# Performance work log

Hardware: AMD Instinct MI355X
Metric: run time of the kernel (lower is better)

The kernel has to match this reference:

```python
import jax, jax.numpy as jnp
import numpy as np

DIM = 256
H = W = 56
WS = 7           # window size
SHIFT = 3        # shift size
NH = 8           # num heads
HD = DIM // NH   # head dim
N = WS * WS      # tokens per window
SCALE = HD ** -0.5
EPS = 1e-5


def _rel_pos_index():
    coords = np.stack(np.meshgrid(np.arange(WS), np.arange(WS), indexing='ij'))  # (2,WS,WS)
    cf = coords.reshape(2, -1)                                # (2, N)
    rel = cf[:, :, None] - cf[:, None, :]                     # (2, N, N)
    rel = rel.transpose(1, 2, 0).astype(np.int64)             # (N, N, 2)
    rel[:, :, 0] += WS - 1
    rel[:, :, 1] += WS - 1
    rel[:, :, 0] *= 2 * WS - 1
    return rel.sum(-1)                                        # (N, N)

REL_IDX = _rel_pos_index()


def _attn_mask():
    # standard Swin shift mask: (nW, N, N) with 0 / -100
    img = np.zeros((H, W))
    cnt = 0
    for hs in (slice(0, -WS), slice(-WS, -SHIFT), slice(-SHIFT, None)):
        for ws in (slice(0, -WS), slice(-WS, -SHIFT), slice(-SHIFT, None)):
            img[hs, ws] = cnt
            cnt += 1
    win = img.reshape(H // WS, WS, W // WS, WS).transpose(0, 2, 1, 3).reshape(-1, N)  # (nW, N)
    diff = win[:, None, :] - win[:, :, None]
    return np.where(diff != 0, -100.0, 0.0).astype(np.float32)

ATTN_MASK = jnp.asarray(_attn_mask())  # (nW, N, N)


def _ln(x, g, b):
    mu = jnp.mean(x, -1, keepdims=True)
    var = jnp.mean(jnp.square(x - mu), -1, keepdims=True)
    return (x - mu) * jax.lax.rsqrt(var + EPS) * g + b


def _win_part(x):
    # (B,H,W,C) -> (B*nW, N, C)
    B, _, _, C = x.shape
    x = x.reshape(B, H // WS, WS, W // WS, WS, C)
    return x.transpose(0, 1, 3, 2, 4, 5).reshape(-1, N, C)


def _win_rev(xw, B):
    # (B*nW, N, C) -> (B,H,W,C)
    C = xw.shape[-1]
    x = xw.reshape(B, H // WS, W // WS, WS, WS, C)
    return x.transpose(0, 1, 3, 2, 4, 5).reshape(B, H, W, C)


def setup_inputs() -> dict:
    key = jax.random.key(0)
    ks = jax.random.split(key, 6)
    return {
        'x': jax.random.normal(ks[0], (32, H * W, DIM), jnp.float32),
        'norm1_g': jnp.ones((DIM,), jnp.float32),
        'norm1_b': jnp.zeros((DIM,), jnp.float32),
        'qkv_w': jax.random.normal(ks[1], (3 * DIM, DIM), jnp.float32) * 0.02,
        'qkv_b': jnp.zeros((3 * DIM,), jnp.float32),
        'rel_table': jax.random.normal(ks[2], ((2 * WS - 1) ** 2, NH), jnp.float32) * 0.02,
        'proj_w': jax.random.normal(ks[3], (DIM, DIM), jnp.float32) * 0.02,
        'proj_b': jnp.zeros((DIM,), jnp.float32),
        'norm2_g': jnp.ones((DIM,), jnp.float32),
        'norm2_b': jnp.zeros((DIM,), jnp.float32),
        'fc1_w': jax.random.normal(ks[4], (4 * DIM, DIM), jnp.float32) * 0.02,
        'fc1_b': jnp.zeros((4 * DIM,), jnp.float32),
        'fc2_w': jax.random.normal(ks[5], (DIM, 4 * DIM), jnp.float32) * 0.02,
        'fc2_b': jnp.zeros((DIM,), jnp.float32),
    }


def reference(x, norm1_g, norm1_b, qkv_w, qkv_b, rel_table, proj_w, proj_b,
              norm2_g, norm2_b, fc1_w, fc1_b, fc2_w, fc2_b):
    B = x.shape[0]
    shortcut = x
    h = _ln(x, norm1_g, norm1_b).reshape(B, H, W, DIM)
    # cyclic shift
    h = jnp.roll(h, (-SHIFT, -SHIFT), axis=(1, 2))
    xw = _win_part(h)                                  # (B*nW, N, C)
    Bw = xw.shape[0]
    qkv = (xw @ qkv_w.T + qkv_b).reshape(Bw, N, 3, NH, HD).transpose(2, 0, 3, 1, 4)
    q, k, v = qkv[0] * SCALE, qkv[1], qkv[2]           # (Bw, NH, N, HD)
    attn = jnp.einsum('bhnd,bhmd->bhnm', q, k)         # (Bw, NH, N, N)
    bias = rel_table[REL_IDX.reshape(-1)].reshape(N, N, NH).transpose(2, 0, 1)
    attn = attn + bias[None]
    nW = ATTN_MASK.shape[0]
    attn = attn.reshape(B, nW, NH, N, N) + ATTN_MASK[None, :, None]
    attn = jax.nn.softmax(attn.reshape(Bw, NH, N, N), axis=-1)
    out = jnp.einsum('bhnm,bhmd->bhnd', attn, v).transpose(0, 2, 1, 3).reshape(Bw, N, DIM)
    out = out @ proj_w.T + proj_b
    h = _win_rev(out, B)
    h = jnp.roll(h, (SHIFT, SHIFT), axis=(1, 2)).reshape(B, H * W, DIM)
    x = shortcut + h
    y = _ln(x, norm2_g, norm2_b)
    y = jax.nn.gelu(y @ fc1_w.T + fc1_b, approximate=False)
    y = y @ fc2_w.T + fc2_b
    return x + y
```

## Files before the change

### kernel.cpp

```cpp
#include <hip/hip_runtime.h>


typedef float f4 __attribute__((ext_vector_type(4)));
typedef __bf16 b8 __attribute__((ext_vector_type(8)));

#define DEV static __device__ __forceinline__

DEV ushort f2bf(float f) {
  union { float f; unsigned u; } c; c.f = f;
  unsigned u = c.u;
  u += 0x7fffu + ((u >> 16) & 1u);
  return (ushort)(u >> 16);
}
DEV __bf16 bfb(ushort u) { union { ushort u; __bf16 b; } c; c.u = u; return c.b; }
DEV b8 zero_b8() {
  b8 z;
#pragma unroll
  for (int i = 0; i < 8; ++i) z[i] = (__bf16)0.f;
  return z;
}
DEV void load_lds16(const void* g, void* l) {
  __builtin_amdgcn_global_load_lds(
      (const __attribute__((address_space(1))) unsigned int*)g,
      (__attribute__((address_space(3))) unsigned int*)l, 16, 0, 0);
}
DEV int reg3(int t) { return t < 49 ? 0 : (t < 53 ? 1 : 2); }

__global__ __launch_bounds__(256) void cast_w(const float* a, ushort* oa, int na,
                                              const float* b, ushort* ob, int nb,
                                              const float* c, ushort* oc, int nc,
                                              const float* d, ushort* od, int nd) {
  int total = na + nb + nc + nd;
  for (int i = blockIdx.x * 256 + threadIdx.x; i < total; i += gridDim.x * 256) {
    int j = i;
    if (j < na) { oa[j] = f2bf(a[j]); continue; }
    j -= na;
    if (j < nb) { ob[j] = f2bf(b[j]); continue; }
    j -= nb;
    if (j < nc) { oc[j] = f2bf(c[j]); continue; }
    j -= nc;
    od[j] = f2bf(d[j]);
  }
}

__global__ __launch_bounds__(256) void build_bias(const float* __restrict__ rel_table,
                                                  float* __restrict__ comb) {
  const int idx = blockIdx.x * 256 + threadIdx.x;
  if (idx >= 4 * 8 * 64 * 64) return;
  const int j = idx & 63, i = (idx >> 6) & 63, h = (idx >> 12) & 7, ty = idx >> 15;
  float v;
  if (i < 49 && j < 49) {
    const int iy = i / 7, ix = i - iy * 7, jy = j / 7, jx = j - jy * 7;
    const int ridx = (iy - jy + 6) * 13 + (ix - jx + 6);
    v = rel_table[ridx * 8 + h];
    const int wh = (ty & 2) ? 7 : 0, ww = (ty & 1) ? 7 : 0;
    const int irg = reg3(wh * 7 + iy) * 3 + reg3(ww * 7 + ix);
    const int jrg = reg3(wh * 7 + jy) * 3 + reg3(ww * 7 + jx);
    if (irg != jrg) v -= 100.f;
  } else {
    v = -1e30f;
  }
  comb[idx] = v;
}

__global__ __launch_bounds__(256) void ln_shift(const float* __restrict__ x,
                                                const float* __restrict__ g,
                                                const float* __restrict__ bta,
                                                ushort* __restrict__ out, int shifted) {
  const int wid = threadIdx.x >> 6, lane = threadIdx.x & 63;
  const int t = blockIdx.x * 4 + wid;
  int src;
  if (shifted) {
    int win = t / 49, n = t - win * 49;
    int bb = win >> 6, wh = (win >> 3) & 7, ww = win & 7;
    int wy = n / 7, wx = n - wy * 7;
    int r = wh * 7 + wy + 3; if (r >= 56) r -= 56;
    int c = ww * 7 + wx + 3; if (c >= 56) c -= 56;
    src = bb * 3136 + r * 56 + c;
  } else {
    src = t;
  }
  const float4 v = *(const float4*)(x + (size_t)src * 256 + lane * 4);
  float s  = v.x + v.y + v.z + v.w;
  float s2 = v.x * v.x + v.y * v.y + v.z * v.z + v.w * v.w;
#pragma unroll
  for (int m = 32; m; m >>= 1) { s += __shfl_xor(s, m); s2 += __shfl_xor(s2, m); }
  const float mean = s * (1.f / 256.f);
  const float var  = s2 * (1.f / 256.f) - mean * mean;
  const float rs   = rsqrtf(var + 1e-5f);
  const float4 gv = *(const float4*)(g + lane * 4);
  const float4 bv = *(const float4*)(bta + lane * 4);
  ushort4 o;
  o.x = f2bf((v.x - mean) * rs * gv.x + bv.x);
  o.y = f2bf((v.y - mean) * rs * gv.y + bv.y);
  o.z = f2bf((v.z - mean) * rs * gv.z + bv.z);
  o.w = f2bf((v.w - mean) * rs * gv.w + bv.w);
  *(ushort4*)(out + (size_t)t * 256 + lane * 4) = o;
}

template <class Epi>
__global__ __launch_bounds__(256) void gemm_bt(const ushort* __restrict__ A,
                                               const ushort* __restrict__ B,
                                               int K, int NT, Epi epi) {
  __shared__ ushort lsA[3][128 * 32];
  __shared__ ushort lsB[3][128 * 32];
  const int tid = threadIdx.x;
  const int lane = tid & 63, wid = tid >> 6;
  const int quad = lane >> 4, l16 = lane & 15;
  const int wm = wid >> 1, wn = wid & 1;
  const int lin = blockIdx.x;
  const int xcd = lin & 7, j = lin >> 3;
  const int mt = xcd * 98 + j / NT;
  const int nt_ = j % NT;
  const long rowA0 = (long)mt * 128;
  const long colB0 = (long)nt_ * 128;
  f4 acc[4][4];
#pragma unroll
  for (int i = 0; i < 4; ++i)
#pragma unroll
    for (int jj = 0; jj < 4; ++jj) { acc[i][jj][0] = 0.f; acc[i][jj][1] = 0.f; acc[i][jj][2] = 0.f; acc[i][jj][3] = 0.f; }
  const int lrow = lane >> 2;
  const int lk = ((lane & 3) ^ ((lane >> 3) & 3)) * 8;
  const int rsw = (quad ^ ((l16 >> 1) & 3)) * 8;
  const int seg0 = wid * 2, seg1 = wid * 2 + 1;
  const long ga0 = (rowA0 + seg0 * 16 + lrow) * (long)K + lk;
  const long ga1 = (rowA0 + seg1 * 16 + lrow) * (long)K + lk;
  const long gb0 = (colB0 + seg0 * 16 + lrow) * (long)K + lk;
  const long gb1 = (colB0 + seg1 * 16 + lrow) * (long)K + lk;

  const int nsteps = K >> 5;
#pragma unroll
  for (int p = 0; p < 3; ++p) {
    const int kk = p << 5;
    load_lds16(A + ga0 + kk, &lsA[p][seg0 * 512]);
    load_lds16(A + ga1 + kk, &lsA[p][seg1 * 512]);
    load_lds16(B + gb0 + kk, &lsB[p][seg0 * 512]);
    load_lds16(B + gb1 + kk, &lsB[p][seg1 * 512]);
  }
  asm volatile("s_waitcnt vmcnt(8)" ::: "memory");
  __builtin_amdgcn_s_barrier();

  int cur = 0;
  for (int t = 0; t < nsteps; ++t) {
    b8 af[4], bfr[4];
#pragma unroll
    for (int ti = 0; ti < 4; ++ti)
      af[ti] = *(const b8*)&lsA[cur][(wm * 64 + ti * 16 + l16) * 32 + rsw];
#pragma unroll
    for (int tj = 0; tj < 4; ++tj)
      bfr[tj] = *(const b8*)&lsB[cur][(wn * 64 + tj * 16 + l16) * 32 + rsw];
#pragma unroll
    for (int ti = 0; ti < 4; ++ti)
#pragma unroll
      for (int tj = 0; tj < 4; ++tj)
        acc[ti][tj] = __builtin_amdgcn_mfma_f32_16x16x32_bf16(af[ti], bfr[tj], acc[ti][tj], 0, 0, 0);
    __builtin_amdgcn_s_barrier();
    if (t + 3 < nsteps) {
      const int kk = (t + 3) << 5;
      load_lds16(A + ga0 + kk, &lsA[cur][seg0 * 512]);
      load_lds16(A + ga1 + kk, &lsA[cur][seg1 * 512]);
      load_lds16(B + gb0 + kk, &lsB[cur][seg0 * 512]);
      load_lds16(B + gb1 + kk, &lsB[cur][seg1 * 512]);
      asm volatile("s_waitcnt vmcnt(8)" ::: "memory");
    } else if (t + 2 < nsteps) {
      asm volatile("s_waitcnt vmcnt(4)" ::: "memory");
    } else if (t + 1 < nsteps) {
      asm volatile("s_waitcnt vmcnt(0)" ::: "memory");
    }
    __builtin_amdgcn_s_barrier();
    cur = cur == 2 ? 0 : cur + 1;
  }
#pragma unroll
  for (int ti = 0; ti < 4; ++ti)
#pragma unroll
    for (int tj = 0; tj < 4; ++tj)
#pragma unroll
      for (int r = 0; r < 4; ++r)
        epi((int)(rowA0 + wm * 64 + ti * 16 + quad * 4 + r),
            (int)(colB0 + wn * 64 + tj * 16 + l16), acc[ti][tj][r]);
}

struct QkvEpi {
  ushort* out; const float* bias;
  __device__ void operator()(int r, int c, float v) const {
    v += bias[c];
    if (c < 256) v *= 0.17677669529663687f;
    out[(size_t)r * 768 + c] = f2bf(v);
  }
};
struct GeluEpi {
  ushort* out; const float* bias;
  __device__ void operator()(int r, int c, float v) const {
    v += bias[c];
    v = 0.5f * v * (1.f + erff(v * 0.70710678118654752f));
    out[(size_t)r * 1024 + c] = f2bf(v);
  }
};
struct Fc2Epi {
  float* out; const float* bias;
  __device__ void operator()(int r, int c, float v) const {
    size_t i = (size_t)r * 256 + c;
    out[i] = out[i] + v + bias[c];
  }
};

__global__ __launch_bounds__(512) void attn_proj(const ushort* __restrict__ qkv,
                                                 const float* __restrict__ comb,
                                                 const ushort* __restrict__ projw,
                                                 const float* __restrict__ projb,
                                                 const float* __restrict__ x_in,
                                                 const float* __restrict__ n2g,
                                                 const float* __restrict__ n2b,
                                                 float* __restrict__ x_out,
                                                 ushort* __restrict__ xw2) {
  __shared__ ushort sbuf[32768];
  const int win = blockIdx.x;
  const int b = win >> 6, wh = (win >> 3) & 7, ww = win & 7;
  const int tid = threadIdx.x, lane = tid & 63, h = tid >> 6;
  const int quad = lane >> 4, l16 = lane & 15;
  const size_t wbase = (size_t)win * 49 * 768;

  b8 af[4], bfr[4];
#pragma unroll
  for (int ti = 0; ti < 4; ++ti) {
    const int tok = ti * 16 + l16;
    af[ti] = (tok < 49) ? *(const b8*)(qkv + wbase + (size_t)tok * 768 + h * 32 + quad * 8)
                        : zero_b8();
  }
#pragma unroll
  for (int tj = 0; tj < 4; ++tj) {
    const int key = tj * 16 + l16;
    bfr[tj] = (key < 49) ? *(const b8*)(qkv + wbase + (size_t)key * 768 + 256 + h * 32 + quad * 8)
                         : zero_b8();
  }
  f4 S[4][4];
#pragma unroll
  for (int ti = 0; ti < 4; ++ti)
#pragma unroll
    for (int tj = 0; tj < 4; ++tj) {
      S[ti][tj][0] = 0.f; S[ti][tj][1] = 0.f; S[ti][tj][2] = 0.f; S[ti][tj][3] = 0.f;
      S[ti][tj] = __builtin_amdgcn_mfma_f32_16x16x32_bf16(af[ti], bfr[tj], S[ti][tj], 0, 0, 0);
    }

  ushort* P = sbuf + h * 4096;
  const float* cmb = comb + ((((wh == 7) ? 2 : 0) + ((ww == 7) ? 1 : 0)) * 8 + h) * 4096;
#pragma unroll
  for (int ti = 0; ti < 4; ++ti) {
#pragma unroll
    for (int r = 0; r < 4; ++r) {
      const int i = ti * 16 + quad * 4 + r;
      const float* crow = cmb + i * 64 + l16;
      float sv[4];
#pragma unroll
      for (int tj = 0; tj < 4; ++tj) sv[tj] = S[ti][tj][r] + crow[tj * 16];
      float m = fmaxf(fmaxf(sv[0], sv[1]), fmaxf(sv[2], sv[3]));
#pragma unroll
      for (int d = 1; d < 16; d <<= 1) m = fmaxf(m, __shfl_xor(m, d));
      float sum = 0.f;
#pragma unroll
      for (int tj = 0; tj < 4; ++tj) { sv[tj] = __expf(sv[tj] - m); sum += sv[tj]; }
#pragma unroll
      for (int d = 1; d < 16; d <<= 1) sum += __shfl_xor(sum, d);
      const float inv = 1.f / sum;
      const int swz = i & 7, off = l16 & 7, cb = l16 >> 3;
#pragma unroll
      for (int tj = 0; tj < 4; ++tj) {
        const int cc = tj * 2 + cb;
        P[i * 64 + (((cc ^ swz) << 3) | off)] = f2bf(sv[tj] * inv);
      }
    }
  }

  f4 O[4][2];
#pragma unroll
  for (int ti = 0; ti < 4; ++ti)
#pragma unroll
    for (int tn = 0; tn < 2; ++tn) { O[ti][tn][0] = 0.f; O[ti][tn][1] = 0.f; O[ti][tn][2] = 0.f; O[ti][tn][3] = 0.f; }
#pragma unroll
  for (int kt = 0; kt < 2; ++kt) {
    b8 vb[2];
#pragma unroll
    for (int tn = 0; tn < 2; ++tn)
#pragma unroll
      for (int j = 0; j < 8; ++j) {
        const int key = kt * 32 + quad * 8 + j;
        vb[tn][j] = (key < 49)
            ? bfb(qkv[wbase + (size_t)key * 768 + 512 + h * 32 + tn * 16 + l16])
            : (__bf16)0.f;
      }
#pragma unroll
    for (int ti = 0; ti < 4; ++ti) {
      const int row = ti * 16 + l16;
      const b8 pa = *(const b8*)(P + row * 64 + (((kt * 4 + quad) ^ (row & 7)) << 3));
#pragma unroll
      for (int tn = 0; tn < 2; ++tn)
        O[ti][tn] = __builtin_amdgcn_mfma_f32_16x16x32_bf16(pa, vb[tn], O[ti][tn], 0, 0, 0);
    }
  }

  __syncthreads();
  ushort* ob = sbuf;
#pragma unroll
  for (int ti = 0; ti < 4; ++ti)
#pragma unroll
    for (int tn = 0; tn < 2; ++tn)
#pragma unroll
      for (int r = 0; r < 4; ++r) {
        const int tok = ti * 16 + quad * 4 + r;
        const int cc = h * 4 + tn * 2 + (l16 >> 3);
        ob[tok * 256 + (((cc ^ (tok & 7)) << 3) | (l16 & 7))] = f2bf(O[ti][tn][r]);
      }
  __syncthreads();

  f4 C[4][2];
#pragma unroll
  for (int ti = 0; ti < 4; ++ti)
#pragma unroll
    for (int tn = 0; tn < 2; ++tn) { C[ti][tn][0] = 0.f; C[ti][tn][1] = 0.f; C[ti][tn][2] = 0.f; C[ti][tn][3] = 0.f; }
  for (int k0 = 0; k0 < 256; k0 += 32) {
    b8 bw[2];
#pragma unroll
    for (int tn = 0; tn < 2; ++tn)
      bw[tn] = *(const b8*)(projw + (size_t)(h * 32 + tn * 16 + l16) * 256 + k0 + quad * 8);
#pragma unroll
    for (int ti = 0; ti < 4; ++ti) {
      const int row = ti * 16 + l16;
      const b8 pa = *(const b8*)(ob + row * 256 + ((((k0 >> 3) + quad) ^ (row & 7)) << 3));
#pragma unroll
      for (int tn = 0; tn < 2; ++tn)
        C[ti][tn] = __builtin_amdgcn_mfma_f32_16x16x32_bf16(pa, bw[tn], C[ti][tn], 0, 0, 0);
    }
  }

  __syncthreads();
  float* fbuf = (float*)sbuf;
#pragma unroll
  for (int ti = 0; ti < 4; ++ti)
#pragma unroll
    for (int r = 0; r < 4; ++r) {
      const int tok = ti * 16 + quad * 4 + r;
      const int swz = tok & 7;
#pragma unroll
      for (int tn = 0; tn < 2; ++tn) {
        const int c4 = h * 8 + tn * 4 + (l16 >> 2);
        fbuf[tok * 256 + (((c4 ^ swz) << 2) | (l16 & 3))] = C[ti][tn][r];
      }
    }
  __syncthreads();

  for (int t = h; t < 49; t += 8) {
    const int wy = t / 7, wx = t - wy * 7;
    int rr = wh * 7 + wy + 3; if (rr >= 56) rr -= 56;
    int cc = ww * 7 + wx + 3; if (cc >= 56) cc -= 56;
    const size_t base = ((size_t)b * 3136 + rr * 56 + cc) * 256;
    float4 v = *(float4*)&fbuf[t * 256 + ((lane ^ (t & 7)) << 2)];
    const float4 pb = *(const float4*)(projb + lane * 4);
    const float4 xr = *(const float4*)(x_in + base + lane * 4);
    v.x += pb.x + xr.x; v.y += pb.y + xr.y; v.z += pb.z + xr.z; v.w += pb.w + xr.w;
    *(float4*)(x_out + base + lane * 4) = v;
    float s  = v.x + v.y + v.z + v.w;
    float s2 = v.x * v.x + v.y * v.y + v.z * v.z + v.w * v.w;
#pragma unroll
    for (int m = 32; m; m >>= 1) { s += __shfl_xor(s, m); s2 += __shfl_xor(s2, m); }
    const float mean = s * (1.f / 256.f);
    const float var  = s2 * (1.f / 256.f) - mean * mean;
    const float rs   = rsqrtf(var + 1e-5f);
    const float4 gv = *(const float4*)(n2g + lane * 4);
    const float4 bv = *(const float4*)(n2b + lane * 4);
    ushort4 o;
    o.x = f2bf((v.x - mean) * rs * gv.x + bv.x);
    o.y = f2bf((v.y - mean) * rs * gv.y + bv.y);
    o.z = f2bf((v.z - mean) * rs * gv.z + bv.z);
    o.w = f2bf((v.w - mean) * rs * gv.w + bv.w);
    *(ushort4*)(xw2 + base + lane * 4) = o;
  }
}

extern "C" void kernel_launch(void* const* d_in, const int* in_sizes, int n_in,
                              void* d_out, int out_size, void* d_ws, size_t ws_size,
                              hipStream_t stream) {
  const float* x     = (const float*)d_in[0];
  const float* n1g   = (const float*)d_in[1];
  const float* n1b   = (const float*)d_in[2];
  const float* qkvw  = (const float*)d_in[3];
  const float* qkvb  = (const float*)d_in[4];
  const float* relt  = (const float*)d_in[5];
  const float* projw = (const float*)d_in[6];
  const float* projb = (const float*)d_in[7];
  const float* n2g   = (const float*)d_in[8];
  const float* n2b   = (const float*)d_in[9];
  const float* fc1w  = (const float*)d_in[10];
  const float* fc1b  = (const float*)d_in[11];
  const float* fc2w  = (const float*)d_in[12];
  const float* fc2b  = (const float*)d_in[13];
  float* out = (float*)d_out;
  char* ws = (char*)d_ws;

  ushort* xw     = (ushort*)ws;
  ushort* qkv    = (ushort*)(ws + 51380224);
  ushort* hidden = qkv;
  float*  comb   = (float*)(ws + 205520896);
  ushort* wqkv   = (ushort*)(ws + 51380224 + 205520896);
  ushort* wproj  = wqkv + 196608;
  ushort* wfc1   = wproj + 65536;
  ushort* wfc2   = wfc1 + 262144;

  cast_w<<<768, 256, 0, stream>>>(qkvw, wqkv, 196608, projw, wproj, 65536,
                                  fc1w, wfc1, 262144, fc2w, wfc2, 262144);
  build_bias<<<512, 256, 0, stream>>>(relt, comb);
  ln_shift<<<25088, 256, 0, stream>>>(x, n1g, n1b, xw, 1);
  gemm_bt<<<4704, 256, 0, stream>>>(xw, wqkv, 256, 6, QkvEpi{qkv, qkvb});
  attn_proj<<<2048, 512, 0, stream>>>(qkv, comb, wproj, projb, x, n2g, n2b, out, xw);
  gemm_bt<<<6272, 256, 0, stream>>>(xw, wfc1, 256, 8, GeluEpi{hidden, fc1b});
  gemm_bt<<<1568, 256, 0, stream>>>(hidden, wfc2, 1024, 2, Fc2Epi{out, fc2b});
}
```

Before: 693.3 us.

## Switch GEMMs to 256x256 tiles with 8 waves and 4-stage split prefetch

Replaces the 128x128, 4-wave GEMM with a 256x256-tile, 512-thread kernel. It uses 128KB of dynamic LDS holding four buffers, which gives a prefetch depth of three. Each K-step is split into two MFMA halves, with the A and B prefetches interleaved between them and s_setprio raised around the MFMA bursts. The larger tile cuts global and LDS traffic per flop, at the cost of fewer blocks: fc2 now gets only 392 blocks, and the LDS footprint limits occupancy to one block per CU.

Result: slower. 710.4 us (+2.5%).

```diff
diff --git a/kernel.cpp b/kernel.cpp
--- a/kernel.cpp
+++ b/kernel.cpp
@@ -99,26 +99,27 @@
 }
 
 template <class Epi>
-__global__ __launch_bounds__(256) void gemm_bt(const ushort* __restrict__ A,
-                                               const ushort* __restrict__ B,
-                                               int K, int NT, Epi epi) {
-  __shared__ ushort lsA[3][128 * 32];
-  __shared__ ushort lsB[3][128 * 32];
+__global__ __launch_bounds__(512, 2) void gemm256(const ushort* __restrict__ A,
+                                                  const ushort* __restrict__ B,
+                                                  int K, int NT, Epi epi) {
+  extern __shared__ __align__(16) ushort smem[];
+  ushort* lsA = smem;
+  ushort* lsB = smem + 4 * 8192;
   const int tid = threadIdx.x;
   const int lane = tid & 63, wid = tid >> 6;
   const int quad = lane >> 4, l16 = lane & 15;
-  const int wm = wid >> 1, wn = wid & 1;
+  const int wm = wid >> 2, wn = wid & 3;
   const int lin = blockIdx.x;
-  const int xcd = lin & 7, j = lin >> 3;
-  const int mt = xcd * 98 + j / NT;
-  const int nt_ = j % NT;
-  const long rowA0 = (long)mt * 128;
-  const long colB0 = (long)nt_ * 128;
-  f4 acc[4][4];
-#pragma unroll
-  for (int i = 0; i < 4; ++i)
-#pragma unroll
-    for (int jj = 0; jj < 4; ++jj) { acc[i][jj][0] = 0.f; acc[i][jj][1] = 0.f; acc[i][jj][2] = 0.f; acc[i][jj][3] = 0.f; }
+  const int xcd = lin & 7, jj = lin >> 3;
+  const int mt = xcd * 49 + jj / NT;
+  const int nt_ = jj % NT;
+  const long rowA0 = (long)mt * 256;
+  const long colB0 = (long)nt_ * 256;
+  f4 acc[8][4];
+#pragma unroll
+  for (int i = 0; i < 8; ++i)
+#pragma unroll
+    for (int j = 0; j < 4; ++j) { acc[i][j][0] = 0.f; acc[i][j][1] = 0.f; acc[i][j][2] = 0.f; acc[i][j][3] = 0.f; }
   const int lrow = lane >> 2;
   const int lk = ((lane & 3) ^ ((lane >> 3) & 3)) * 8;
   const int rsw = (quad ^ ((l16 >> 1) & 3)) * 8;
@@ -131,36 +132,56 @@
   const int nsteps = K >> 5;
 #pragma unroll
   for (int p = 0; p < 3; ++p) {
-    const int kk = p << 5;
-    load_lds16(A + ga0 + kk, &lsA[p][seg0 * 512]);
-    load_lds16(A + ga1 + kk, &lsA[p][seg1 * 512]);
-    load_lds16(B + gb0 + kk, &lsB[p][seg0 * 512]);
-    load_lds16(B + gb1 + kk, &lsB[p][seg1 * 512]);
+    const int bo = p * 8192, kk = p << 5;
+    load_lds16(A + ga0 + kk, lsA + bo + seg0 * 512);
+    load_lds16(A + ga1 + kk, lsA + bo + seg1 * 512);
+    load_lds16(B + gb0 + kk, lsB + bo + seg0 * 512);
+    load_lds16(B + gb1 + kk, lsB + bo + seg1 * 512);
   }
   asm volatile("s_waitcnt vmcnt(8)" ::: "memory");
   __builtin_amdgcn_s_barrier();
 
-  int cur = 0;
   for (int t = 0; t < nsteps; ++t) {
+    const ushort* bufA = lsA + (t & 3) * 8192;
+    const ushort* bufB = lsB + (t & 3) * 8192;
+    const int sbo = ((t + 3) & 3) * 8192, skk = (t + 3) << 5;
+    if (t + 3 < nsteps) {
+      load_lds16(A + ga0 + skk, lsA + sbo + seg0 * 512);
+      load_lds16(A + ga1 + skk, lsA + sbo + seg1 * 512);
+    }
     b8 af[4], bfr[4];
 #pragma unroll
     for (int ti = 0; ti < 4; ++ti)
-      af[ti] = *(const b8*)&lsA[cur][(wm * 64 + ti * 16 + l16) * 32 + rsw];
+      af[ti] = *(const b8*)&bufA[(wm * 128 + ti * 16 + l16) * 32 + rsw];
 #pragma unroll
     for (int tj = 0; tj < 4; ++tj)
-      bfr[tj] = *(const b8*)&lsB[cur][(wn * 64 + tj * 16 + l16) * 32 + rsw];
+      bfr[tj] = *(const b8*)&bufB[(wn * 64 + tj * 16 + l16) * 32 + rsw];
+    __builtin_amdgcn_s_barrier();
+    __builtin_amdgcn_s_setprio(1);
 #pragma unroll
     for (int ti = 0; ti < 4; ++ti)
 #pragma unroll
       for (int tj = 0; tj < 4; ++tj)
         acc[ti][tj] = __builtin_amdgcn_mfma_f32_16x16x32_bf16(af[ti], bfr[tj], acc[ti][tj], 0, 0, 0);
+    __builtin_amdgcn_s_setprio(0);
     __builtin_amdgcn_s_barrier();
     if (t + 3 < nsteps) {
-      const int kk = (t + 3) << 5;
-      load_lds16(A + ga0 + kk, &lsA[cur][seg0 * 512]);
-      load_lds16(A + ga1 + kk, &lsA[cur][seg1 * 512]);
-      load_lds16(B + gb0 + kk, &lsB[cur][seg0 * 512]);
-      load_lds16(B + gb1 + kk, &lsB[cur][seg1 * 512]);
+      load_lds16(B + gb0 + skk, lsB + sbo + seg0 * 512);
+      load_lds16(B + gb1 + skk, lsB + sbo + seg1 * 512);
+    }
+    b8 af2[4];
+#pragma unroll
+    for (int ti = 0; ti < 4; ++ti)
+      af2[ti] = *(const b8*)&bufA[(wm * 128 + (4 + ti) * 16 + l16) * 32 + rsw];
+    __builtin_amdgcn_s_barrier();
+    __builtin_amdgcn_s_setprio(1);
+#pragma unroll
+    for (int ti = 0; ti < 4; ++ti)
+#pragma unroll
+      for (int tj = 0; tj < 4; ++tj)
+        acc[4 + ti][tj] = __builtin_amdgcn_mfma_f32_16x16x32_bf16(af2[ti], bfr[tj], acc[4 + ti][tj], 0, 0, 0);
+    __builtin_amdgcn_s_setprio(0);
+    if (t + 3 < nsteps) {
       asm volatile("s_waitcnt vmcnt(8)" ::: "memory");
     } else if (t + 2 < nsteps) {
       asm volatile("s_waitcnt vmcnt(4)" ::: "memory");
@@ -168,15 +189,14 @@
       asm volatile("s_waitcnt vmcnt(0)" ::: "memory");
     }
     __builtin_amdgcn_s_barrier();
-    cur = cur == 2 ? 0 : cur + 1;
-  }
-#pragma unroll
-  for (int ti = 0; ti < 4; ++ti)
+  }
+#pragma unroll
+  for (int ti = 0; ti < 8; ++ti)
 #pragma unroll
     for (int tj = 0; tj < 4; ++tj)
 #pragma unroll
       for (int r = 0; r < 4; ++r)
-        epi((int)(rowA0 + wm * 64 + ti * 16 + quad * 4 + r),
+        epi((int)(rowA0 + wm * 128 + ti * 16 + quad * 4 + r),
             (int)(colB0 + wn * 64 + tj * 16 + l16), acc[ti][tj][r]);
 }
 
@@ -405,12 +425,23 @@
   ushort* wfc1   = wproj + 65536;
   ushort* wfc2   = wfc1 + 262144;
 
+  static bool attr_done = false;
+  if (!attr_done) {
+    attr_done = true;
+    hipFuncSetAttribute(reinterpret_cast<const void*>(&gemm256<QkvEpi>),
+                        hipFuncAttributeMaxDynamicSharedMemorySize, 131072);
+    hipFuncSetAttribute(reinterpret_cast<const void*>(&gemm256<GeluEpi>),
+                        hipFuncAttributeMaxDynamicSharedMemorySize, 131072);
+    hipFuncSetAttribute(reinterpret_cast<const void*>(&gemm256<Fc2Epi>),
+                        hipFuncAttributeMaxDynamicSharedMemorySize, 131072);
+  }
+
   cast_w<<<768, 256, 0, stream>>>(qkvw, wqkv, 196608, projw, wproj, 65536,
                                   fc1w, wfc1, 262144, fc2w, wfc2, 262144);
   build_bias<<<512, 256, 0, stream>>>(relt, comb);
   ln_shift<<<25088, 256, 0, stream>>>(x, n1g, n1b, xw, 1);
-  gemm_bt<<<4704, 256, 0, stream>>>(xw, wqkv, 256, 6, QkvEpi{qkv, qkvb});
+  gemm256<<<1176, 512, 131072, stream>>>(xw, wqkv, 256, 3, QkvEpi{qkv, qkvb});
   attn_proj<<<2048, 512, 0, stream>>>(qkv, comb, wproj, projb, x, n2g, n2b, out, xw);
-  gemm_bt<<<6272, 256, 0, stream>>>(xw, wfc1, 256, 8, GeluEpi{hidden, fc1b});
-  gemm_bt<<<1568, 256, 0, stream>>>(hidden, wfc2, 1024, 2, Fc2Epi{out, fc2b});
-}
+  gemm256<<<1568, 512, 131072, stream>>>(xw, wfc1, 256, 4, GeluEpi{hidden, fc1b});
+  gemm256<<<392, 512, 131072, stream>>>(hidden, wfc2, 1024, 1, Fc2Epi{out, fc2b});
+}
```
